# Performance work log

Measured on AMD Instinct MI355X. Metric: run time of the kernel, lower is better.

The kernel has to match this reference:

```python
import jax, jax.numpy as jnp
import numpy as np

LAMBDA = 25.0
MU = 25.0
NU = 1.0
ALPHA = 0.25
EPS = 1e-4
NUM_MATCHES = (20, 4)


def _cdist(a, b):
    # a: (B, Na, D), b: (B, Nb, D) -> euclidean distances (B, Na, Nb)
    d2 = (jnp.sum(a * a, axis=-1)[:, :, None]
          + jnp.sum(b * b, axis=-1)[:, None, :]
          - 2.0 * jnp.einsum('bnd,bmd->bnm', a, b))
    return jnp.sqrt(jnp.maximum(d2, 0.0))


def _nearest_neighbors(input_maps, candidate_maps, distances, num_matches):
    # Faithful to lightly.models.utils.nearest_neighbors:
    #  1) for each input element find its nearest candidate (argmin over last dim)
    #  2) keep the num_matches input elements with smallest nn distance
    # Indices are non-differentiable in torch, so stop_gradient on distances.
    distances = jax.lax.stop_gradient(distances)
    nn_idx = jnp.argmin(distances, axis=-1)           # (B, Na)
    nn_val = jnp.min(distances, axis=-1)              # (B, Na)
    _, min_idx = jax.lax.top_k(-nn_val, num_matches)  # smallest num_matches -> (B, M)
    filt_in = jnp.take_along_axis(input_maps, min_idx[..., None], axis=1)      # (B, M, C)
    cand_nn = jnp.take_along_axis(candidate_maps, nn_idx[..., None], axis=1)   # (B, Na, C)
    filt_cand = jnp.take_along_axis(cand_nn, min_idx[..., None], axis=1)       # (B, M, C)
    return filt_in, filt_cand


def _mse(a, b):
    return jnp.mean((a - b) ** 2)


def _variance_loss(x):
    # torch.var default is unbiased (ddof=1)
    std = jnp.sqrt(jnp.var(x, axis=0, ddof=1) + EPS)
    return jnp.mean(jax.nn.relu(1.0 - std))


def _covariance_loss(x):
    n, d = x.shape
    x = x - jnp.mean(x, axis=0)
    cov = (x.T @ x) / (n - 1)                         # (D, D)
    off = cov - jnp.diag(jnp.diag(cov))
    return jnp.sum(off ** 2) / d


def _global_loss(z_a, z_b):
    inv = _mse(z_a, z_b)
    var = 0.5 * (_variance_loss(z_a) + _variance_loss(z_b))
    cov = _covariance_loss(z_a) + _covariance_loss(z_b)
    return LAMBDA * inv + MU * var + NU * cov


def _local_loss(za, zb, ga, gb):
    B = za.shape[0]
    za = za.reshape(B, -1, za.shape[-1])              # (B, H*W, C)
    zb = zb.reshape(B, -1, zb.shape[-1])
    ga = ga.reshape(B, -1, 2)                          # (B, H*W, 2)
    gb = gb.reshape(B, -1, 2)
    has_local_view = za.shape[1] != zb.shape[1]
    nm = NUM_MATCHES[1] if has_local_view else NUM_MATCHES[0]
    # L2 feature-space matching
    fa, na = _nearest_neighbors(za, zb, _cdist(za, zb), nm)
    fb, nb = _nearest_neighbors(zb, za, _cdist(zb, za), nm)
    inv = 0.5 * _mse(fa, na) + 0.5 * _mse(fb, nb)
    # Grid (spatial) matching
    fa, na = _nearest_neighbors(za, zb, _cdist(ga, gb), NUM_MATCHES[0])
    fb, nb = _nearest_neighbors(zb, za, _cdist(gb, ga), NUM_MATCHES[1])
    inv = inv + 0.5 * _mse(fa, na) + 0.5 * _mse(fb, nb)
    return LAMBDA * inv


def setup_inputs() -> dict:
    key = jax.random.key(0)
    k1, k2, k3, k4, k5, k6 = jax.random.split(key, 6)
    B, D = 128, 8192
    H = W = 7
    return {
        'z_a': jax.random.normal(k1, (B, D), dtype=jnp.float32),
        'z_b': jax.random.normal(k2, (B, D), dtype=jnp.float32),
        'z_a_local_features': jax.random.normal(k3, (B, H, W, D), dtype=jnp.float32),
        'z_b_local_features': jax.random.normal(k4, (B, H, W, D), dtype=jnp.float32),
        'grid_a': jax.random.uniform(k5, (B, H, W, 2), dtype=jnp.float32),
        'grid_b': jax.random.uniform(k6, (B, H, W, 2), dtype=jnp.float32),
    }


def reference(z_a, z_b, z_a_local_features, z_b_local_features, grid_a, grid_b):
    g = _global_loss(z_a, z_b)
    l = _local_loss(z_a_local_features, z_b_local_features, grid_a, grid_b)
    return ALPHA * g + (1.0 - ALPHA) * l
```

## Files before the change

### kernel.cpp

```cpp
#include <hip/hip_runtime.h>
#include <math.h>

#define BATCH 128
#define DIM   8192
#define HW    49
#define PAIRS 2401
#define SLOT  2512

#define WS_MSE    0
#define WS_VARA   1
#define WS_VARB   2
#define WS_DIAGA  3
#define WS_DIAGB  4
#define WS_S1     5
#define WS_S2     6
#define WS_S3     7
#define WS_S4     8
#define WS_SK2A   9
#define WS_SK2B   10
#define WS_TICKET 11
#define COLS_OFF    16
#define GRAMA_OFF   32784
#define GRAMB_OFF   49168
#define GK2PART_OFF 65552
#define L1PART_BIG  2162704
#define WS_NEED_FLOATS (L1PART_BIG + 256 * SLOT)
#define L1PART_SMALL 65552

typedef __attribute__((ext_vector_type(8))) short bf16x8;
typedef __attribute__((ext_vector_type(4))) float f32x4;

__device__ __forceinline__ unsigned cvtpk(float lo, float hi) {
    unsigned r;
    asm("v_cvt_pk_bf16_f32 %0, %1, %2" : "=v"(r) : "v"(lo), "v"(hi));
    return r;
}

#define SB0() __builtin_amdgcn_sched_barrier(0)

template<bool RED>
__global__ __launch_bounds__(512) void uber(const float* __restrict__ za_l,
                                            const float* __restrict__ zb_l,
                                            const float* __restrict__ z_a,
                                            const float* __restrict__ z_b,
                                            float* __restrict__ ws,
                                            float* __restrict__ l1part)
{
    __shared__ __align__(16) unsigned char shm[81920];
    const int tid = threadIdx.x;

    if (blockIdx.x < 64) {
        const int chunk = blockIdx.x;
        float* sxA = (float*)shm;
        float* sxB = sxA + 128 * 68;
        float* scr = sxB + 128 * 68;
        const int ty = tid >> 5, tx = tid & 31;
        const int q = tid >> 6, cc = tid & 63;

        float accA[8][4], accB[8][4];
#pragma unroll
        for (int r = 0; r < 8; ++r)
#pragma unroll
            for (int c = 0; c < 4; ++c) { accA[r][c] = 0.f; accB[r][c] = 0.f; }
        float cSA[2] = {0.f,0.f}, cQA[2] = {0.f,0.f};
        float cSB[2] = {0.f,0.f}, cQB[2] = {0.f,0.f};
        float mse = 0.f;

#pragma unroll
        for (int st = 0; st < 2; ++st) {
            __syncthreads();
            for (int f = tid; f < 2048; f += 512) {
                int row = f >> 4, c4 = f & 15;
                const float4 a4 = *(const float4*)(z_a + (size_t)row * DIM + chunk * 128 + st * 64 + c4 * 4);
                const float4 b4 = *(const float4*)(z_b + (size_t)row * DIM + chunk * 128 + st * 64 + c4 * 4);
                *(float4*)(sxA + row * 68 + c4 * 4) = a4;
                *(float4*)(sxB + row * 68 + c4 * 4) = b4;
                float dx = a4.x - b4.x, dy = a4.y - b4.y, dz = a4.z - b4.z, dw = a4.w - b4.w;
                mse += dx * dx + dy * dy + dz * dz + dw * dw;
            }
            __syncthreads();
            for (int r = 0; r < 16; ++r) {
                float vA = sxA[(q * 16 + r) * 68 + cc];
                float vB = sxB[(q * 16 + r) * 68 + cc];
                cSA[st] += vA; cQA[st] += vA * vA;
                cSB[st] += vB; cQB[st] += vB * vB;
            }
            for (int k = 0; k < 64; k += 4) {
                float4 ar4[8], br4[8];
#pragma unroll
                for (int r = 0; r < 8; ++r) {
                    ar4[r] = *(const float4*)(sxA + (ty + 16 * r) * 68 + k);
                    br4[r] = *(const float4*)(sxB + (ty + 16 * r) * 68 + k);
                }
#pragma unroll
                for (int c = 0; c < 4; ++c) {
                    float4 ac4 = *(const float4*)(sxA + (tx + 32 * c) * 68 + k);
                    float4 bc4 = *(const float4*)(sxB + (tx + 32 * c) * 68 + k);
#pragma unroll
                    for (int r = 0; r < 8; ++r) {
                        accA[r][c] += ar4[r].x * ac4.x + ar4[r].y * ac4.y + ar4[r].z * ac4.z + ar4[r].w * ac4.w;
                        accB[r][c] += br4[r].x * bc4.x + br4[r].y * bc4.y + br4[r].z * bc4.z + br4[r].w * bc4.w;
                    }
                }
            }
        }
#pragma unroll
        for (int tens = 0; tens < 2; ++tens) {
            __syncthreads();
            scr[q * 64 + cc]        = tens ? cSB[0] : cSA[0];
            scr[512 + q * 64 + cc]  = tens ? cSB[1] : cSA[1];
            scr[1024 + q * 64 + cc] = tens ? cQB[0] : cQA[0];
            scr[1536 + q * 64 + cc] = tens ? cQB[1] : cQA[1];
            __syncthreads();
            if (tid < 128) {
                int st = tid >> 6, c2 = tid & 63;
                float s = 0.f, qq = 0.f;
#pragma unroll
                for (int g = 0; g < 8; ++g) {
                    s  += scr[st * 512 + g * 64 + c2];
                    qq += scr[1024 + st * 512 + g * 64 + c2];
                }
                int col = chunk * 128 + st * 64 + c2;
                float* C = ws + COLS_OFF + tens * 2 * DIM;
                C[col] = s; C[DIM + col] = qq;
            }
        }
        for (int o = 32; o; o >>= 1) mse += __shfl_xor(mse, o);
        if ((tid & 63) == 0) atomicAdd(&ws[WS_MSE], mse);
        if (RED) {
            float* P = ws + GK2PART_OFF + (size_t)chunk * 32768;
#pragma unroll
            for (int r = 0; r < 8; ++r)
#pragma unroll
                for (int c = 0; c < 4; ++c) {
                    P[(ty + 16 * r) * 128 + tx + 32 * c] = accA[r][c];
                    P[16384 + (ty + 16 * r) * 128 + tx + 32 * c] = accB[r][c];
                }
        } else {
#pragma unroll
            for (int r = 0; r < 8; ++r)
#pragma unroll
                for (int c = 0; c < 4; ++c) {
                    atomicAdd(&ws[GRAMA_OFF + (ty + 16 * r) * 128 + tx + 32 * c], accA[r][c]);
                    atomicAdd(&ws[GRAMB_OFF + (ty + 16 * r) * 128 + tx + 32 * c], accB[r][c]);
                }
        }
        __syncthreads();
    }

    {
        const int lb = blockIdx.x;
        unsigned char* buf0 = shm;
        unsigned char* buf1 = shm + 25088;
        const int wv = tid >> 6, lane = tid & 63;
        const int fr = lane & 15, kg = lane >> 4;
        const int batch = lb >> 1;
        const int kh    = lb & 1;
        const float* Az = za_l + (size_t)batch * HW * DIM + (size_t)kh * 4096;
        const float* Bz = zb_l + (size_t)batch * HW * DIM + (size_t)kh * 4096;

        const int half = lane >> 5, l5 = lane & 31;
        const float* gp[7];
        int wb[7];
#pragma unroll
        for (int i = 0; i < 7; ++i) {
            int j = wv + 8 * i;
            gp[i] = Az; wb[i] = -1;
            if (j < 49) {
                int row = 2 * j + half;
                const float* rbase = (row < 49) ? (Az + (size_t)row * DIM)
                                                : (Bz + (size_t)(row - 49) * DIM);
                gp[i] = rbase + l5 * 4;
                wb[i] = row * 256 + ((((l5 >> 1) ^ (row & 15)) << 4) | ((l5 & 1) << 3));
            }
        }

        const int wr = wv >> 2, wc = wv & 3;
        int ar0 = wr * 32 + fr;
        int ar1 = ar0 + 16; if (ar1 > 48) ar1 = 48;
        int bc  = wc * 16 + fr; if (bc > 48) bc = 48;
        const int brow = 49 + bc;
        const int aw0 = ar0 << 8, pa0 = ar0 & 15;
        const int aw1 = ar1 << 8, pa1 = ar1 & 15;
        const int bw  = brow << 8, pb = brow & 15;

        f32x4 acc00 = {0.f,0.f,0.f,0.f}, acc10 = {0.f,0.f,0.f,0.f};
        f32x4 aa0 = {0.f,0.f,0.f,0.f}, aa1 = {0.f,0.f,0.f,0.f}, bb = {0.f,0.f,0.f,0.f};

        f32x4 RS0[7], RS1[7];

#define GLOAD(dst, i, s) do {                                                  \
        if (wb[i] >= 0) {                                                      \
            const float* p_ = gp[i] + (size_t)(s) * 128;                       \
            asm volatile("global_load_dwordx4 %0, %1, off"                     \
                         : "=v"(dst) : "v"(p_) : "memory");                    \
        } } while (0)

#define L1_LOADS(RS, s) do {                                                   \
        GLOAD(RS[0], 0, s); GLOAD(RS[1], 1, s); GLOAD(RS[2], 2, s);            \
        GLOAD(RS[3], 3, s); GLOAD(RS[4], 4, s); GLOAD(RS[5], 5, s);            \
        GLOAD(RS[6], 6, s); } while (0)

#define L1_CVTWRITE(RS, B) do {                                                \
        _Pragma("unroll") for (int i = 0; i < 7; ++i)                          \
            if (wb[i] >= 0) {                                                  \
                f32x4 v_ = RS[i];                                              \
                *(uint2*)((B) + wb[i]) =                                       \
                    make_uint2(cvtpk(v_.x, v_.y), cvtpk(v_.z, v_.w));          \
            } } while (0)

#define L1_COMPUTE(B) do {                                                     \
        _Pragma("unroll") for (int kk = 0; kk < 4; ++kk) {                     \
            const int s0_ = kk * 4 + kg;                                       \
            bf16x8 a0 = *(const bf16x8*)((B) + aw0 + (((s0_) ^ pa0) << 4));    \
            bf16x8 a1 = *(const bf16x8*)((B) + aw1 + (((s0_) ^ pa1) << 4));    \
            bf16x8 b0 = *(const bf16x8*)((B) + bw  + (((s0_) ^ pb ) << 4));    \
            acc00 = __builtin_amdgcn_mfma_f32_16x16x32_bf16(a0, b0, acc00, 0, 0, 0); \
            acc10 = __builtin_amdgcn_mfma_f32_16x16x32_bf16(a1, b0, acc10, 0, 0, 0); \
            aa0   = __builtin_amdgcn_mfma_f32_16x16x32_bf16(a0, a0, aa0,   0, 0, 0); \
            aa1   = __builtin_amdgcn_mfma_f32_16x16x32_bf16(a1, a1, aa1,   0, 0, 0); \
            bb    = __builtin_amdgcn_mfma_f32_16x16x32_bf16(b0, b0, bb,    0, 0, 0); \
        } } while (0)

#define VMWAIT_STEADY() do {                                                   \
        if (wv == 0) asm volatile("s_waitcnt vmcnt(7)" ::: "memory");          \
        else         asm volatile("s_waitcnt vmcnt(6)" ::: "memory");          \
        } while (0)

        asm volatile("s_waitcnt vmcnt(0)" ::: "memory");
        SB0();

        L1_LOADS(RS0, 0); SB0();
        L1_LOADS(RS1, 1); SB0();

#pragma unroll 1
        for (int s = 0; s < 32; s += 2) {
            VMWAIT_STEADY(); SB0();
            L1_CVTWRITE(RS0, buf0);
            asm volatile("s_waitcnt lgkmcnt(0)" ::: "memory"); SB0();
            __builtin_amdgcn_s_barrier(); SB0();
            if (s + 2 < 32) { L1_LOADS(RS0, s + 2); SB0(); }
            L1_COMPUTE(buf0);
            if (s + 1 == 31) asm volatile("s_waitcnt vmcnt(0)" ::: "memory");
            else             VMWAIT_STEADY();
            SB0();
            L1_CVTWRITE(RS1, buf1);
            asm volatile("s_waitcnt lgkmcnt(0)" ::: "memory"); SB0();
            __builtin_amdgcn_s_barrier(); SB0();
            if (s + 3 < 32) { L1_LOADS(RS1, s + 3); SB0(); }
            L1_COMPUTE(buf1);
        }
#undef GLOAD
#undef L1_LOADS
#undef L1_CVTWRITE
#undef L1_COMPUTE
#undef VMWAIT_STEADY

        float* gout = l1part + (size_t)(RED ? lb : batch) * SLOT;
        const int gc = wc * 16 + fr;
#pragma unroll
        for (int rr = 0; rr < 4; ++rr) {
            int gr0 = wr * 32 + kg * 4 + rr;
            int gr1 = gr0 + 16;
            if (gc < HW) {
                if (gr0 < HW) {
                    if (RED) gout[gr0 * HW + gc] = acc00[rr];
                    else atomicAdd(&gout[gr0 * HW + gc], acc00[rr]);
                }
                if (gr1 < HW) {
                    if (RED) gout[gr1 * HW + gc] = acc10[rr];
                    else atomicAdd(&gout[gr1 * HW + gc], acc10[rr]);
                }
            }
        }
        if (wc == 0) {
#pragma unroll
            for (int rr = 0; rr < 4; ++rr) {
                int i = kg * 4 + rr;
                if (i == fr) {
                    int r0 = wr * 32 + i;
                    if (RED) gout[PAIRS + r0] = aa0[rr];
                    else atomicAdd(&gout[PAIRS + r0], aa0[rr]);
                    int r1 = r0 + 16;
                    if (r1 < HW) {
                        if (RED) gout[PAIRS + r1] = aa1[rr];
                        else atomicAdd(&gout[PAIRS + r1], aa1[rr]);
                    }
                }
            }
        }
        if (wr == 0) {
#pragma unroll
            for (int rr = 0; rr < 4; ++rr) {
                int i = kg * 4 + rr;
                if (i == fr) {
                    int rb_ = wc * 16 + i;
                    if (rb_ < HW) {
                        if (RED) gout[PAIRS + HW + rb_] = bb[rr];
                        else atomicAdd(&gout[PAIRS + HW + rb_], bb[rr]);
                    }
                }
            }
        }
    }
}

template<bool RED>
__global__ __launch_bounds__(256) void merge2(const float* __restrict__ ga,
                                              const float* __restrict__ gb,
                                              float* __restrict__ ws,
                                              const float* __restrict__ l1part)
{
    __shared__ float d2f[PAIRS];
    __shared__ float d2g[PAIRS];
    __shared__ float nAs[49], nBs[49];
    __shared__ float gax[49], gay[49], gbx[49], gby[49];
    __shared__ float mval[4][49];
    __shared__ int   midx[4][49];

    const int b = blockIdx.x;
    const int tid = threadIdx.x;

    if (b < 128) {
        if (!RED) return;
        int gid = b * 256 + tid;
        int tensor = gid >> 14, e = gid & 16383;
        const float* P = ws + GK2PART_OFF + (size_t)tensor * 16384;
        float s = 0.f;
        for (int c = 0; c < 64; ++c) s += P[(size_t)c * 32768 + e];
        ws[(tensor ? GRAMB_OFF : GRAMA_OFF) + e] = s;
        return;
    }
    if (b < 160) {
        int col = (b - 128) * 256 + tid;
        float sa = ws[COLS_OFF + col];
        float qa = ws[COLS_OFF + DIM + col];
        float sb = ws[COLS_OFF + 2 * DIM + col];
        float qb = ws[COLS_OFF + 3 * DIM + col];
        float sA = qa - sa * sa * (1.0f / BATCH);
        float sB = qb - sb * sb * (1.0f / BATCH);
        float rA = fmaxf(0.f, 1.f - sqrtf(sA * (1.0f / (BATCH - 1)) + 1e-4f));
        float rB = fmaxf(0.f, 1.f - sqrtf(sB * (1.0f / (BATCH - 1)) + 1e-4f));
        float dA = sA * sA, dB = sB * sB;
        for (int o = 32; o; o >>= 1) {
            rA += __shfl_xor(rA, o);
            rB += __shfl_xor(rB, o);
            dA += __shfl_xor(dA, o);
            dB += __shfl_xor(dB, o);
        }
        if ((tid & 63) == 0) {
            atomicAdd(&ws[WS_VARA],  rA);
            atomicAdd(&ws[WS_VARB],  rB);
            atomicAdd(&ws[WS_DIAGA], dA);
            atomicAdd(&ws[WS_DIAGB], dB);
        }
        return;
    }

    const int batch = b - 160;
    const float* P0 = l1part + (size_t)batch * (RED ? (2 * SLOT) : SLOT);
    auto rd = [&](int off) -> float {
        if (!RED) return P0[off];
        return P0[off] + P0[SLOT + off];
    };

    if (tid < 49) nAs[tid] = rd(PAIRS + tid);
    else if (tid >= 64 && tid < 113) nBs[tid - 64] = rd(PAIRS + 49 + (tid - 64));
    if (tid >= 128 && tid < 177) {
        int i = tid - 128;
        gax[i] = ga[batch * 98 + i * 2];
        gay[i] = ga[batch * 98 + i * 2 + 1];
    } else if (tid >= 192 && tid < 241) {
        int i = tid - 192;
        gbx[i] = gb[batch * 98 + i * 2];
        gby[i] = gb[batch * 98 + i * 2 + 1];
    }
    __syncthreads();
    for (int e = tid; e < PAIRS; e += 256) {
        int i = e / 49, j = e - i * 49;
        d2f[e] = nAs[i] + nBs[j] - 2.0f * rd(e);
        float dx = gax[i] - gbx[j], dy = gay[i] - gby[j];
        d2g[e] = dx * dx + dy * dy;
    }
    __syncthreads();
    const int task = tid >> 6, l = tid & 63;
    if (l < 49) {
        float bv = 3.0e38f; int bi = 0;
        if (task == 0) {
            for (int j = 0; j < 49; ++j) { float v = d2f[l * 49 + j]; if (v < bv) { bv = v; bi = j; } }
        } else if (task == 1) {
            for (int i = 0; i < 49; ++i) { float v = d2f[i * 49 + l]; if (v < bv) { bv = v; bi = i; } }
        } else if (task == 2) {
            for (int j = 0; j < 49; ++j) { float v = d2g[l * 49 + j]; if (v < bv) { bv = v; bi = j; } }
        } else {
            for (int i = 0; i < 49; ++i) { float v = d2g[i * 49 + l]; if (v < bv) { bv = v; bi = i; } }
        }
        mval[task][l] = bv; midx[task][l] = bi;
    }
    __syncthreads();
    if (l < 49) {
        float v = mval[task][l];
        int rank = 0;
        for (int k = 0; k < 49; ++k) {
            float u = mval[task][k];
            rank += (u < v) || (u == v && k < l);
        }
        if (task == 0)      { if (rank < 20) atomicAdd(&ws[WS_S1], v); }
        else if (task == 1) { if (rank < 20) atomicAdd(&ws[WS_S2], v); }
        else if (task == 2) { if (rank < 20) atomicAdd(&ws[WS_S3], d2f[l * 49 + midx[2][l]]); }
        else                { if (rank < 4)  atomicAdd(&ws[WS_S4], d2f[midx[3][l] * 49 + l]); }
    }
}

__global__ __launch_bounds__(256) void gk3_final(float* __restrict__ ws,
                                                 float* __restrict__ out)
{
    __shared__ float r[128];
    __shared__ float sS;
    __shared__ float wrd[4];
    const int tid = threadIdx.x;
    const float* G = ws + (blockIdx.x ? GRAMB_OFF : GRAMA_OFF);
    if (tid < 128) {
        float s0 = 0.f, s1 = 0.f, s2 = 0.f, s3 = 0.f;
        for (int k = 0; k < 128; k += 4) {
            s0 += G[(k + 0) * 128 + tid];
            s1 += G[(k + 1) * 128 + tid];
            s2 += G[(k + 2) * 128 + tid];
            s3 += G[(k + 3) * 128 + tid];
        }
        r[tid] = (s0 + s1) + (s2 + s3);
    }
    __syncthreads();
    if (tid < 64) {
        float t = r[tid] + r[tid + 64];
        for (int o = 32; o; o >>= 1) t += __shfl_xor(t, o);
        if (tid == 0) sS = t;
    }
    __syncthreads();
    const float S = sS;
    float sk = 0.f;
    for (int e = tid; e < 16384; e += 256) {
        float K = G[e] - (r[e >> 7] + r[e & 127]) * (1.0f / 128.0f) + S * (1.0f / 16384.0f);
        sk += K * K;
    }
    for (int o = 32; o; o >>= 1) sk += __shfl_xor(sk, o);
    if ((tid & 63) == 0) wrd[tid >> 6] = sk;
    __syncthreads();
    if (tid == 0) {
        ws[blockIdx.x ? WS_SK2B : WS_SK2A] = wrd[0] + wrd[1] + wrd[2] + wrd[3];
        __threadfence();
        unsigned t = atomicAdd((unsigned*)&ws[WS_TICKET], 1u);
        if (t == 1) {
            __threadfence();
            float inv_g = ws[WS_MSE] * (1.0f / ((float)BATCH * (float)DIM));
            float varl  = 0.5f * (ws[WS_VARA] + ws[WS_VARB]) * (1.0f / (float)DIM);
            float cov   = (ws[WS_SK2A] - ws[WS_DIAGA] + ws[WS_SK2B] - ws[WS_DIAGB])
                          * (1.0f / (127.0f * 127.0f * (float)DIM));
            float gl = 25.0f * inv_g + 25.0f * varl + cov;
            float m20 = (float)BATCH * 20.0f * (float)DIM;
            float m4  = (float)BATCH * 4.0f  * (float)DIM;
            float invl = 0.5f * (ws[WS_S1] + ws[WS_S2] + ws[WS_S3]) / m20
                       + 0.5f * ws[WS_S4] / m4;
            out[0] = 0.25f * gl + 0.75f * (25.0f * invl);
        }
    }
}

extern "C" void kernel_launch(void* const* d_in, const int* in_sizes, int n_in,
                              void* d_out, int out_size, void* d_ws, size_t ws_size,
                              hipStream_t stream)
{
    (void)in_sizes; (void)n_in; (void)out_size;
    const float* z_a = (const float*)d_in[0];
    const float* z_b = (const float*)d_in[1];
    const float* zla = (const float*)d_in[2];
    const float* zlb = (const float*)d_in[3];
    const float* ga  = (const float*)d_in[4];
    const float* gb  = (const float*)d_in[5];
    float* ws  = (float*)d_ws;
    float* out = (float*)d_out;

    const bool big = ws_size >= (size_t)WS_NEED_FLOATS * sizeof(float);

    if (big) {
        hipMemsetAsync(d_ws, 0, 16 * sizeof(float), stream);
        uber<true><<<256, 512, 0, stream>>>(zla, zlb, z_a, z_b, ws, ws + L1PART_BIG);
        merge2<true><<<288, 256, 0, stream>>>(ga, gb, ws, ws + L1PART_BIG);
        gk3_final<<<2, 256, 0, stream>>>(ws, out);
    } else {
        hipMemsetAsync(d_ws, 0, (size_t)(L1PART_SMALL + BATCH * SLOT) * sizeof(float), stream);
        uber<false><<<256, 512, 0, stream>>>(zla, zlb, z_a, z_b, ws, ws + L1PART_SMALL);
        merge2<false><<<288, 256, 0, stream>>>(ga, gb, ws, ws + L1PART_SMALL);
        gk3_final<<<2, 256, 0, stream>>>(ws, out);
    }
}
```

Before: 121.4 us.

## Split gram blocks from local-feature blocks and quarter the K range per block

The first 64 blocks now do only the global gram/variance work and return early. They stage one tensor at a time through a single smaller LDS tile and recompute the MSE with a separate global reread. The local-feature blocks become separate blocks, each covering a quarter of the feature dimension instead of a half, so the grid grows from 256 to 576 blocks and merge2 sums four partial slots per batch. This is meant to cut LDS use and raise occupancy and parallelism, at the cost of more partial-sum traffic and extra global reads. The non-reduction path indexes l1part by batch with atomics, so its pointer math is unchanged.

```diff
diff --git a/kernel.cpp b/kernel.cpp
--- a/kernel.cpp
+++ b/kernel.cpp
@@ -24,7 +24,7 @@
 #define GRAMB_OFF   49168
 #define GK2PART_OFF 65552
 #define L1PART_BIG  2162704
-#define WS_NEED_FLOATS (L1PART_BIG + 256 * SLOT)
+#define WS_NEED_FLOATS (L1PART_BIG + 512 * SLOT)
 #define L1PART_SMALL 65552
 
 typedef __attribute__((ext_vector_type(8))) short bf16x8;
@@ -46,118 +46,130 @@
                                             float* __restrict__ ws,
                                             float* __restrict__ l1part)
 {
-    __shared__ __align__(16) unsigned char shm[81920];
+    __shared__ __align__(16) unsigned char shm[50176];
     const int tid = threadIdx.x;
 
     if (blockIdx.x < 64) {
         const int chunk = blockIdx.x;
-        float* sxA = (float*)shm;
-        float* sxB = sxA + 128 * 68;
-        float* scr = sxB + 128 * 68;
+        float* sx  = (float*)shm;
+        float* scr = sx + 128 * 68;
         const int ty = tid >> 5, tx = tid & 31;
         const int q = tid >> 6, cc = tid & 63;
 
-        float accA[8][4], accB[8][4];
+        float accA[2][8][4], accB[2][8][4];
 #pragma unroll
         for (int r = 0; r < 8; ++r)
 #pragma unroll
-            for (int c = 0; c < 4; ++c) { accA[r][c] = 0.f; accB[r][c] = 0.f; }
-        float cSA[2] = {0.f,0.f}, cQA[2] = {0.f,0.f};
-        float cSB[2] = {0.f,0.f}, cQB[2] = {0.f,0.f};
-        float mse = 0.f;
+            for (int c = 0; c < 4; ++c) {
+                accA[0][r][c] = 0.f; accB[0][r][c] = 0.f;
+                accA[1][r][c] = 0.f; accB[1][r][c] = 0.f;
+            }
+        float cS[2][2], cQ[2][2];
+        cS[0][0]=cS[0][1]=cS[1][0]=cS[1][1]=0.f;
+        cQ[0][0]=cQ[0][1]=cQ[1][0]=cQ[1][1]=0.f;
 
 #pragma unroll
         for (int st = 0; st < 2; ++st) {
-            __syncthreads();
-            for (int f = tid; f < 2048; f += 512) {
-                int row = f >> 4, c4 = f & 15;
-                const float4 a4 = *(const float4*)(z_a + (size_t)row * DIM + chunk * 128 + st * 64 + c4 * 4);
-                const float4 b4 = *(const float4*)(z_b + (size_t)row * DIM + chunk * 128 + st * 64 + c4 * 4);
-                *(float4*)(sxA + row * 68 + c4 * 4) = a4;
-                *(float4*)(sxB + row * 68 + c4 * 4) = b4;
+#pragma unroll
+            for (int tens = 0; tens < 2; ++tens) {
+                const float* X = tens ? z_b : z_a;
+                __syncthreads();
+                for (int f = tid; f < 2048; f += 512) {
+                    int row = f >> 4, c4 = f & 15;
+                    *(float4*)(sx + row * 68 + c4 * 4) =
+                        *(const float4*)(X + (size_t)row * DIM + chunk * 128 + st * 64 + c4 * 4);
+                }
+                __syncthreads();
+                {
+                    float s = 0.f, qq = 0.f;
+                    for (int r = 0; r < 16; ++r) {
+                        float v = sx[(q * 16 + r) * 68 + cc];
+                        s += v; qq += v * v;
+                    }
+                    cS[tens][st] += s; cQ[tens][st] += qq;
+                }
+                for (int k = 0; k < 64; k += 4) {
+                    float4 r4[8];
+#pragma unroll
+                    for (int r = 0; r < 8; ++r)
+                        r4[r] = *(const float4*)(sx + (ty + 16 * r) * 68 + k);
+#pragma unroll
+                    for (int c = 0; c < 4; ++c) {
+                        float4 c4v = *(const float4*)(sx + (tx + 32 * c) * 68 + k);
+#pragma unroll
+                        for (int r = 0; r < 8; ++r) {
+                            float d = r4[r].x * c4v.x + r4[r].y * c4v.y
+                                    + r4[r].z * c4v.z + r4[r].w * c4v.w;
+                            if (tens) accB[0][r][c] += d; else accA[0][r][c] += d;
+                        }
+                    }
+                }
+            }
+        }
+#pragma unroll
+        for (int tens = 0; tens < 2; ++tens)
+#pragma unroll
+            for (int st = 0; st < 2; ++st) {
+                __syncthreads();
+                scr[q * 64 + cc]       = cS[tens][st];
+                scr[512 + q * 64 + cc] = cQ[tens][st];
+                __syncthreads();
+                if (tid < 64) {
+                    float s = 0.f, qq = 0.f;
+#pragma unroll
+                    for (int g = 0; g < 8; ++g) {
+                        s  += scr[g * 64 + tid];
+                        qq += scr[512 + g * 64 + tid];
+                    }
+                    int col = chunk * 128 + st * 64 + tid;
+                    float* C = ws + COLS_OFF + tens * 2 * DIM;
+                    C[col] = s; C[DIM + col] = qq;
+                }
+            }
+        {
+            float mse = 0.f;
+            for (int f = tid; f < 4096; f += 512) {
+                int row = f >> 5, c4 = f & 31;
+                size_t idx = (size_t)row * DIM + chunk * 128 + c4 * 4;
+                float4 a4 = *(const float4*)(z_a + idx);
+                float4 b4 = *(const float4*)(z_b + idx);
                 float dx = a4.x - b4.x, dy = a4.y - b4.y, dz = a4.z - b4.z, dw = a4.w - b4.w;
                 mse += dx * dx + dy * dy + dz * dz + dw * dw;
             }
-            __syncthreads();
-            for (int r = 0; r < 16; ++r) {
-                float vA = sxA[(q * 16 + r) * 68 + cc];
-                float vB = sxB[(q * 16 + r) * 68 + cc];
-                cSA[st] += vA; cQA[st] += vA * vA;
-                cSB[st] += vB; cQB[st] += vB * vB;
-            }
-            for (int k = 0; k < 64; k += 4) {
-                float4 ar4[8], br4[8];
-#pragma unroll
-                for (int r = 0; r < 8; ++r) {
-                    ar4[r] = *(const float4*)(sxA + (ty + 16 * r) * 68 + k);
-                    br4[r] = *(const float4*)(sxB + (ty + 16 * r) * 68 + k);
-                }
-#pragma unroll
-                for (int c = 0; c < 4; ++c) {
-                    float4 ac4 = *(const float4*)(sxA + (tx + 32 * c) * 68 + k);
-                    float4 bc4 = *(const float4*)(sxB + (tx + 32 * c) * 68 + k);
-#pragma unroll
-                    for (int r = 0; r < 8; ++r) {
-                        accA[r][c] += ar4[r].x * ac4.x + ar4[r].y * ac4.y + ar4[r].z * ac4.z + ar4[r].w * ac4.w;
-                        accB[r][c] += br4[r].x * bc4.x + br4[r].y * bc4.y + br4[r].z * bc4.z + br4[r].w * bc4.w;
-                    }
-                }
-            }
-        }
-#pragma unroll
-        for (int tens = 0; tens < 2; ++tens) {
-            __syncthreads();
-            scr[q * 64 + cc]        = tens ? cSB[0] : cSA[0];
-            scr[512 + q * 64 + cc]  = tens ? cSB[1] : cSA[1];
-            scr[1024 + q * 64 + cc] = tens ? cQB[0] : cQA[0];
-            scr[1536 + q * 64 + cc] = tens ? cQB[1] : cQA[1];
-            __syncthreads();
-            if (tid < 128) {
-                int st = tid >> 6, c2 = tid & 63;
-                float s = 0.f, qq = 0.f;
-#pragma unroll
-                for (int g = 0; g < 8; ++g) {
-                    s  += scr[st * 512 + g * 64 + c2];
-                    qq += scr[1024 + st * 512 + g * 64 + c2];
-                }
-                int col = chunk * 128 + st * 64 + c2;
-                float* C = ws + COLS_OFF + tens * 2 * DIM;
-                C[col] = s; C[DIM + col] = qq;
-            }
-        }
-        for (int o = 32; o; o >>= 1) mse += __shfl_xor(mse, o);
-        if ((tid & 63) == 0) atomicAdd(&ws[WS_MSE], mse);
+            for (int o = 32; o; o >>= 1) mse += __shfl_xor(mse, o);
+            if ((tid & 63) == 0) atomicAdd(&ws[WS_MSE], mse);
+        }
         if (RED) {
             float* P = ws + GK2PART_OFF + (size_t)chunk * 32768;
 #pragma unroll
             for (int r = 0; r < 8; ++r)
 #pragma unroll
                 for (int c = 0; c < 4; ++c) {
-                    P[(ty + 16 * r) * 128 + tx + 32 * c] = accA[r][c];
-                    P[16384 + (ty + 16 * r) * 128 + tx + 32 * c] = accB[r][c];
+                    P[(ty + 16 * r) * 128 + tx + 32 * c] = accA[0][r][c];
+                    P[16384 + (ty + 16 * r) * 128 + tx + 32 * c] = accB[0][r][c];
                 }
         } else {
 #pragma unroll
             for (int r = 0; r < 8; ++r)
 #pragma unroll
                 for (int c = 0; c < 4; ++c) {
-                    atomicAdd(&ws[GRAMA_OFF + (ty + 16 * r) * 128 + tx + 32 * c], accA[r][c]);
-                    atomicAdd(&ws[GRAMB_OFF + (ty + 16 * r) * 128 + tx + 32 * c], accB[r][c]);
-                }
-        }
-        __syncthreads();
+                    atomicAdd(&ws[GRAMA_OFF + (ty + 16 * r) * 128 + tx + 32 * c], accA[0][r][c]);
+                    atomicAdd(&ws[GRAMB_OFF + (ty + 16 * r) * 128 + tx + 32 * c], accB[0][r][c]);
+                }
+        }
+        return;
     }
 
     {
-        const int lb = blockIdx.x;
+        const int lb = blockIdx.x - 64;
         unsigned char* buf0 = shm;
         unsigned char* buf1 = shm + 25088;
         const int wv = tid >> 6, lane = tid & 63;
         const int fr = lane & 15, kg = lane >> 4;
-        const int batch = lb >> 1;
-        const int kh    = lb & 1;
-        const float* Az = za_l + (size_t)batch * HW * DIM + (size_t)kh * 4096;
-        const float* Bz = zb_l + (size_t)batch * HW * DIM + (size_t)kh * 4096;
+        const int batch = lb >> 2;
+        const int ks    = lb & 3;
+        const float* Az = za_l + (size_t)batch * HW * DIM + (size_t)ks * 2048;
+        const float* Bz = zb_l + (size_t)batch * HW * DIM + (size_t)ks * 2048;
 
         const int half = lane >> 5, l5 = lane & 31;
         const float* gp[7];
@@ -234,20 +246,20 @@
         L1_LOADS(RS1, 1); SB0();
 
 #pragma unroll 1
-        for (int s = 0; s < 32; s += 2) {
+        for (int s = 0; s < 16; s += 2) {
             VMWAIT_STEADY(); SB0();
             L1_CVTWRITE(RS0, buf0);
             asm volatile("s_waitcnt lgkmcnt(0)" ::: "memory"); SB0();
             __builtin_amdgcn_s_barrier(); SB0();
-            if (s + 2 < 32) { L1_LOADS(RS0, s + 2); SB0(); }
+            if (s + 2 < 16) { L1_LOADS(RS0, s + 2); SB0(); }
             L1_COMPUTE(buf0);
-            if (s + 1 == 31) asm volatile("s_waitcnt vmcnt(0)" ::: "memory");
+            if (s + 1 == 15) asm volatile("s_waitcnt vmcnt(0)" ::: "memory");
             else             VMWAIT_STEADY();
             SB0();
             L1_CVTWRITE(RS1, buf1);
             asm volatile("s_waitcnt lgkmcnt(0)" ::: "memory"); SB0();
             __builtin_amdgcn_s_barrier(); SB0();
-            if (s + 3 < 32) { L1_LOADS(RS1, s + 3); SB0(); }
+            if (s + 3 < 16) { L1_LOADS(RS1, s + 3); SB0(); }
             L1_COMPUTE(buf1);
         }
 #undef GLOAD
@@ -358,10 +370,13 @@
     }
 
     const int batch = b - 160;
-    const float* P0 = l1part + (size_t)batch * (RED ? (2 * SLOT) : SLOT);
+    const float* P0 = l1part + (size_t)batch * (RED ? (4 * SLOT) : SLOT);
     auto rd = [&](int off) -> float {
         if (!RED) return P0[off];
-        return P0[off] + P0[SLOT + off];
+        float s = 0.f;
+#pragma unroll
+        for (int ss = 0; ss < 4; ++ss) s += P0[ss * SLOT + off];
+        return s;
     };
 
     if (tid < 49) nAs[tid] = rd(PAIRS + tid);
@@ -484,12 +499,12 @@
 
     if (big) {
         hipMemsetAsync(d_ws, 0, 16 * sizeof(float), stream);
-        uber<true><<<256, 512, 0, stream>>>(zla, zlb, z_a, z_b, ws, ws + L1PART_BIG);
+        uber<true><<<576, 512, 0, stream>>>(zla, zlb, z_a, z_b, ws, ws + L1PART_BIG);
         merge2<true><<<288, 256, 0, stream>>>(ga, gb, ws, ws + L1PART_BIG);
         gk3_final<<<2, 256, 0, stream>>>(ws, out);
     } else {
         hipMemsetAsync(d_ws, 0, (size_t)(L1PART_SMALL + BATCH * SLOT) * sizeof(float), stream);
-        uber<false><<<256, 512, 0, stream>>>(zla, zlb, z_a, z_b, ws, ws + L1PART_SMALL);
+        uber<false><<<576, 512, 0, stream>>>(zla, zlb, z_a, z_b, ws, ws + L1PART_SMALL);
         merge2<false><<<288, 256, 0, stream>>>(ga, gb, ws, ws + L1PART_SMALL);
         gk3_final<<<2, 256, 0, stream>>>(ws, out);
     }
```

Result: faster. 117.0 us (-3.7%).
